# Optimization experiments

Hardware: AMD Instinct MI355X
Metric: run time of the kernel (lower is better)

The kernel has to match this reference:

```python
import jax, jax.numpy as jnp
import numpy as np

# Per-species MLP dims from CoefficientLayer._create_model (H, C, N, O), aev_dim=384
DIMS = {"h": [384, 160, 128, 96, 1], "c": [384, 144, 112, 96, 1], "n": [384, 128, 112, 96, 1], "o": [384, 128, 112, 96, 1]}


def setup_inputs() -> dict:
    key = jax.random.key(0)
    B, A, D = 256, 256, 384
    ks = jax.random.split(key, 64)
    inp = {}
    inp["species"] = jax.random.randint(ks[0], (B, A), 0, 4)  # species index 0..3
    inp["aev"] = jax.random.normal(ks[1], (B, A, D), dtype=jnp.float32)
    inp["b0"] = jnp.array([0.1, 0.2, 0.3, 0.4], dtype=jnp.float32)  # shifter intercepts
    inp["b1"] = jnp.array([1.0, 1.1, 0.9, 1.2], dtype=jnp.float32)  # shifter slopes
    ki = 2
    for name, dims in DIMS.items():
        for l in range(4):
            fi, fo = dims[l], dims[l + 1]
            inp[f"{name}w{l}"] = jax.random.normal(ks[ki], (fi, fo), dtype=jnp.float32) / np.float32(np.sqrt(fi))
            ki += 1
            inp[f"{name}b{l}"] = jnp.zeros((fo,), dtype=jnp.float32)
    return inp


def _mlp(x, ws, bs):
    # Linear -> CELU(0.1) x3 -> Linear(->1), squeeze last dim
    for i in range(3):
        x = jax.nn.celu(x @ ws[i] + bs[i], alpha=0.1)
    return (x @ ws[3] + bs[3])[..., 0]


def reference(species, aev, b0, b1,
              hw0, hb0, hw1, hb1, hw2, hb2, hw3, hb3,
              cw0, cb0, cw1, cb1, cw2, cb2, cw3, cb3,
              nw0, nb0, nw1, nb1, nw2, nb2, nw3, nb3,
              ow0, ob0, ow1, ob1, ow2, ob2, ow3, ob3):
    nets = [
        ([hw0, hw1, hw2, hw3], [hb0, hb1, hb2, hb3]),
        ([cw0, cw1, cw2, cw3], [cb0, cb1, cb2, cb3]),
        ([nw0, nw1, nw2, nw3], [nb0, nb1, nb2, nb3]),
        ([ow0, ow1, ow2, ow3], [ob0, ob1, ob2, ob3]),
    ]
    # ANIModel hard routing: each atom's coefficient comes from its species' network;
    # atoms with species == -1 (padding) stay 0.
    coef = jnp.zeros(species.shape, dtype=aev.dtype)
    for i, (ws, bs) in enumerate(nets):  # fixed small loop over 4 species
        coef = jnp.where(species == i, _mlp(aev, ws, bs), coef)
    # Shifter: result[mask_i] = b0[i] + b1[i] * coef[mask_i]; padding stays 0
    idx = jnp.clip(species, 0)
    return jnp.where(species >= 0, b0[idx] + b1[idx] * coef, jnp.zeros((), dtype=aev.dtype))
```

## Files before the change

### kernel.cpp

```cpp
#include <hip/hip_runtime.h>

typedef _Float16 f16;
typedef _Float16 f16x8 __attribute__((ext_vector_type(8)));
typedef float f32x4 __attribute__((ext_vector_type(4)));
typedef unsigned short u16;

#define NATOMS 65536
#define SLOT 10240

#define WS_LISTS_OFF 256
#define WS_W_OFF 524544
#define WS_W_ELEMS 350208
#define WS_NEEDED (WS_W_OFF + WS_W_ELEMS * 2)

struct ConvJob { const float* src; int K, N, KS, NT, CK, off; };

struct PrepParams {
  const int* species;
  int* counts;
  u16* lists;
  f16* wbase;
  ConvJob jobs[16];
};

struct MlpParams {
  const float* aev;
  const float* b0;
  const float* b1;
  const float* bias[4][4];
  const f16* w[4][4];
  const int* counts;
  const u16* lists;
  float* out;
  int Nreal0[4];
  int Nreal1[4];
};

__global__ __launch_bounds__(256) void prep_kernel(PrepParams p) {
  int tid = threadIdx.x;
  if (blockIdx.x < 256) {
    __shared__ int wcnt[4][4];
    __shared__ int wbase[4][4];
    int i = blockIdx.x * 256 + tid;
    int s = p.species[i];
    int wave = tid >> 6, lane = tid & 63;
    unsigned long long m[4];
    #pragma unroll
    for (int t = 0; t < 4; t++) {
      m[t] = __ballot(s == t);
      if (lane == 0) wcnt[wave][t] = __popcll(m[t]);
    }
    __syncthreads();
    if (tid < 4) {
      int t = tid;
      int c0 = wcnt[0][t], c1 = wcnt[1][t], c2 = wcnt[2][t], c3 = wcnt[3][t];
      int base = atomicAdd(&p.counts[t], c0 + c1 + c2 + c3);
      wbase[0][t] = base;
      wbase[1][t] = base + c0;
      wbase[2][t] = base + c0 + c1;
      wbase[3][t] = base + c0 + c1 + c2;
    }
    __syncthreads();
    int rnk = __popcll(m[s] & ((1ull << lane) - 1ull));
    p.lists[s * NATOMS + wbase[wave][s] + rnk] = (u16)i;
  } else {
    int bx = blockIdx.x - 256;
    int job = bx / 30, bxin = bx - job * 30;
    ConvJob jb = p.jobs[job];
    int e = bxin * 256 + tid;
    int nslots = jb.KS * jb.NT * 64;
    if (e >= nslots) return;
    int frag = e >> 6, lane = e & 63;
    int c = frag / (jb.CK * jb.NT);
    int rem = frag - c * (jb.CK * jb.NT);
    int ckc = min(jb.CK, jb.KS - c * jb.CK);
    int nt = rem / ckc, ki = rem - nt * ckc;
    int ks = c * jb.CK + ki;
    int q = lane >> 4, nlo = lane & 15;
    int n = nt * 16 + nlo;
    int k0 = ks * 32 + q * 8;
    f16x8 v;
    #pragma unroll
    for (int j = 0; j < 8; j++) {
      int k = k0 + j;
      float x = (n < jb.N && k < jb.K) ? jb.src[k * jb.N + n] : 0.f;
      v[j] = (f16)x;
    }
    *(f16x8*)(p.wbase + jb.off + (size_t)e * 8) = v;
  }
}

__device__ __forceinline__ float celu01(float v) {
  return v > 0.f ? v : 0.1f * (__expf(v * 10.f) - 1.f);
}

__device__ __forceinline__ void stage_frag(const f16* g, f16* l, int lane) {
  __builtin_amdgcn_global_load_lds(
      (const __attribute__((address_space(1))) unsigned int*)(g + lane * 8),
      (__attribute__((address_space(3))) unsigned int*)l, 16, 0, 0);
}

template <int KS, int NT, int CK>
__device__ __forceinline__ int run_layer(const f16x8* a, const f16* __restrict__ Wt,
                                         const float* __restrict__ bias, int Nreal,
                                         f16* dstw, int DS, f16* ring, int par,
                                         const f16* nextW, int nextNF,
                                         f32x4* acc, int w, int lane, int q, int nlo) {
  constexpr int C = (KS + CK - 1) / CK;
  #pragma unroll
  for (int nt = 0; nt < NT; nt++) acc[nt] = f32x4{0.f, 0.f, 0.f, 0.f};
  #pragma unroll
  for (int c = 0; c < C; c++) {
    f16* cur = ring + par * SLOT;
    f16* nxt = ring + (par ^ 1) * SLOT;
    if (c + 1 < C) {
      const f16* gb = Wt + (size_t)((c + 1) * CK * NT) * 512;
      int nf = min(CK, KS - (c + 1) * CK) * NT;
      for (int f = w; f < nf; f += 4)
        stage_frag(gb + (size_t)f * 512, nxt + f * 512, lane);
    } else if (nextNF > 0) {
      for (int f = w; f < nextNF; f += 4)
        stage_frag(nextW + (size_t)f * 512, nxt + f * 512, lane);
    }
    int ckc = min(CK, KS - c * CK);
    #pragma unroll
    for (int nt = 0; nt < NT; nt++) {
      #pragma unroll
      for (int ki = 0; ki < CK; ki++) {
        if (ki < ckc) {
          f16x8 b = *(const f16x8*)(cur + (nt * ckc + ki) * 512 + lane * 8);
          acc[nt] = __builtin_amdgcn_mfma_f32_16x16x32_f16(a[c * CK + ki], b, acc[nt], 0, 0, 0);
        }
      }
    }
    __syncthreads();
    par ^= 1;
  }
  #pragma unroll
  for (int nt = 0; nt < NT; nt++) {
    int n = nt * 16 + nlo;
    float bv = (n < Nreal) ? bias[n] : 0.f;
    #pragma unroll
    for (int r = 0; r < 4; r++) {
      float v = celu01(acc[nt][r] + bv);
      dstw[(q * 4 + r) * DS + n] = (f16)v;
    }
  }
  return par;
}

template <int NT0, int KS1>
__device__ __forceinline__ void mlp_body(const MlpParams& p, int s, int tile,
                                         f16* ring, f16* Bf0, f16* Bf1) {
  int cnt = p.counts[s];
  if (tile * 64 >= cnt) return;
  const u16* list = p.lists + s * NATOMS;
  int tid = threadIdx.x, w = tid >> 6, lane = tid & 63;
  int q = lane >> 4, nlo = lane & 15;
  int rowbase = tile * 64 + w * 16;
  int atom = list[min(rowbase + nlo, cnt - 1)];

  f16x8 a0[12];
  const float* ap = p.aev + (size_t)atom * 384 + q * 8;
  #pragma unroll
  for (int ks = 0; ks < 12; ks++) {
    float4 u0 = *(const float4*)(ap + ks * 32);
    float4 u1 = *(const float4*)(ap + ks * 32 + 4);
    f16x8 t = {(f16)u0.x, (f16)u0.y, (f16)u0.z, (f16)u0.w,
               (f16)u1.x, (f16)u1.y, (f16)u1.z, (f16)u1.w};
    a0[ks] = t;
  }

  for (int f = w; f < 2 * NT0; f += 4)
    stage_frag(p.w[s][0] + (size_t)f * 512, ring + f * 512, lane);
  __syncthreads();

  f16* my0 = Bf0 + (w * 16) * 168;
  f16* my1 = Bf1 + (w * 16) * 136;
  f32x4 acc[10];

  int par = 0;
  par = run_layer<12, NT0, 2>(a0, p.w[s][0], p.bias[s][0], p.Nreal0[s], my0, 168,
                              ring, par, p.w[s][1], 16, acc, w, lane, q, nlo);

  f16x8 a1[KS1];
  #pragma unroll
  for (int ks = 0; ks < KS1; ks++)
    a1[ks] = *(const f16x8*)(my0 + nlo * 168 + ks * 32 + q * 8);
  par = run_layer<KS1, 8, 2>(a1, p.w[s][1], p.bias[s][1], p.Nreal1[s], my1, 136,
                             ring, par, p.w[s][2], 12, acc, w, lane, q, nlo);

  f16x8 a2[4];
  #pragma unroll
  for (int ks = 0; ks < 4; ks++)
    a2[ks] = *(const f16x8*)(my1 + nlo * 136 + ks * 32 + q * 8);
  par = run_layer<4, 6, 2>(a2, p.w[s][2], p.bias[s][2], 96, my0, 168,
                           ring, par, (const f16*)0, 0, acc, w, lane, q, nlo);

  f16x8 a3[3];
  #pragma unroll
  for (int ks = 0; ks < 3; ks++)
    a3[ks] = *(const f16x8*)(my0 + nlo * 168 + ks * 32 + q * 8);
  f32x4 acc3 = {0.f, 0.f, 0.f, 0.f};
  const f16* W3 = p.w[s][3];
  #pragma unroll
  for (int ks = 0; ks < 3; ks++) {
    f16x8 b = *(const f16x8*)(W3 + (size_t)(ks * 64 + lane) * 8);
    acc3 = __builtin_amdgcn_mfma_f32_16x16x32_f16(a3[ks], b, acc3, 0, 0, 0);
  }
  if (nlo == 0) {
    float b3 = p.bias[s][3][0];
    float b0v = p.b0[s], b1v = p.b1[s];
    #pragma unroll
    for (int r = 0; r < 4; r++) {
      int m = rowbase + q * 4 + r;
      if (m < cnt) {
        float coef = acc3[r] + b3;
        p.out[list[m]] = b0v + b1v * coef;
      }
    }
  }
}

__global__ __launch_bounds__(256, 2) void mlp_kernel(MlpParams p) {
  __shared__ f16 ring[2 * SLOT];
  __shared__ f16 Bf0[64 * 168];
  __shared__ f16 Bf1[64 * 136];
  int s = blockIdx.x & 3;
  int tile = blockIdx.x >> 2;
  switch (s) {
    case 0: mlp_body<10, 5>(p, 0, tile, ring, Bf0, Bf1); break;
    case 1: mlp_body<10, 5>(p, 1, tile, ring, Bf0, Bf1); break;
    case 2: mlp_body<8, 4>(p, 2, tile, ring, Bf0, Bf1); break;
    default: mlp_body<8, 4>(p, 3, tile, ring, Bf0, Bf1); break;
  }
}

extern "C" void kernel_launch(void* const* d_in, const int* in_sizes, int n_in,
                              void* d_out, int out_size, void* d_ws, size_t ws_size,
                              hipStream_t stream) {
  if (ws_size < WS_NEEDED) return;

  const int* species = (const int*)d_in[0];
  const float* aev = (const float*)d_in[1];
  const float* b0 = (const float*)d_in[2];
  const float* b1 = (const float*)d_in[3];

  static const int F1[4]  = {160, 144, 128, 128};
  static const int F1p[4] = {160, 160, 128, 128};
  static const int F2[4]  = {128, 112, 112, 112};

  char* wsb = (char*)d_ws;
  int* counts = (int*)wsb;
  u16* lists = (u16*)(wsb + WS_LISTS_OFF);
  f16* wbase = (f16*)(wsb + WS_W_OFF);

  PrepParams pp;
  pp.species = species; pp.counts = counts; pp.lists = lists; pp.wbase = wbase;

  MlpParams mp;
  mp.aev = aev; mp.b0 = b0; mp.b1 = b1;
  mp.counts = counts; mp.lists = lists; mp.out = (float*)d_out;

  int off = 0, ji = 0;
  for (int s = 0; s < 4; s++) {
    int K[4]  = {384, F1[s], F2[s], 96};
    int N[4]  = {F1[s], F2[s], 96, 1};
    int KS[4] = {12, F1p[s] / 32, 4, 3};
    int NT[4] = {F1p[s] / 16, 8, 6, 1};
    int CK[4] = {2, 2, 2, 3};
    for (int l = 0; l < 4; l++) {
      const float* w = (const float*)d_in[4 + s * 8 + l * 2];
      const float* b = (const float*)d_in[4 + s * 8 + l * 2 + 1];
      pp.jobs[ji].src = w;
      pp.jobs[ji].K = K[l];
      pp.jobs[ji].N = N[l];
      pp.jobs[ji].KS = KS[l];
      pp.jobs[ji].NT = NT[l];
      pp.jobs[ji].CK = CK[l];
      pp.jobs[ji].off = off;
      mp.w[s][l] = wbase + off;
      mp.bias[s][l] = b;
      off += KS[l] * NT[l] * 512;
      ji++;
    }
    mp.Nreal0[s] = F1[s];
    mp.Nreal1[s] = F2[s];
  }

  hipMemsetAsync(d_ws, 0, 64, stream);
  prep_kernel<<<dim3(256 + 480), 256, 0, stream>>>(pp);
  mlp_kernel<<<dim3(280 * 4), 256, 0, stream>>>(mp);
}
```

Measured before the change: 284.1 us.

## Warp-specialize weight staging with a producer wave and flag-synced triple-buffered ring

Adds a dedicated fifth wave that streams all layer weight chunks into a three-slot LDS ring via async global-to-LDS loads, signalling consumers through shared flags and waiting on per-chunk completion counters instead of block-wide barriers. Consumer waves process one K-step per chunk and merge the two activation buffers into one, shrinking LDS to allow more resident blocks. This aims to remove __syncthreads stalls and overlap weight loading across layer boundaries, at the cost of spin-wait polling, atomics, and finer-grained chunks.

```diff
diff --git a/kernel.cpp b/kernel.cpp
--- a/kernel.cpp
+++ b/kernel.cpp
@@ -6,7 +6,8 @@
 typedef unsigned short u16;
 
 #define NATOMS 65536
-#define SLOT 10240
+#define SLOT 5120
+#define RING 3
 
 #define WS_LISTS_OFF 256
 #define WS_W_OFF 524544
@@ -100,41 +101,69 @@
       (__attribute__((address_space(3))) unsigned int*)l, 16, 0, 0);
 }
 
-template <int KS, int NT, int CK>
-__device__ __forceinline__ int run_layer(const f16x8* a, const f16* __restrict__ Wt,
-                                         const float* __restrict__ bias, int Nreal,
-                                         f16* dstw, int DS, f16* ring, int par,
-                                         const f16* nextW, int nextNF,
-                                         f32x4* acc, int w, int lane, int q, int nlo) {
-  constexpr int C = (KS + CK - 1) / CK;
+template <int NT0, int KS1>
+struct Sched {
+  static constexpr int NC = 12 + KS1 + 4 + 1;
+  static constexpr int frags(int c) {
+    return c < 12 ? NT0 : (c < 12 + KS1 ? 8 : (c < 12 + KS1 + 4 ? 6 : 3));
+  }
+};
+
+template <int NT0, int KS1, int C>
+__device__ __forceinline__ void issue_chunk(const f16* w0, const f16* w1,
+                                            const f16* w2, const f16* w3,
+                                            f16* ring, int lane) {
+  constexpr int NF = Sched<NT0, KS1>::frags(C);
+  const f16* g;
+  if constexpr (C < 12) g = w0 + (size_t)C * NT0 * 512;
+  else if constexpr (C < 12 + KS1) g = w1 + (size_t)(C - 12) * 8 * 512;
+  else if constexpr (C < 12 + KS1 + 4) g = w2 + (size_t)(C - 12 - KS1) * 6 * 512;
+  else g = w3;
+  f16* l = ring + (C % RING) * SLOT;
+  #pragma unroll
+  for (int f = 0; f < NF; f++)
+    stage_frag(g + f * 512, l + f * 512, lane);
+}
+
+template <int NT0, int KS1, int C>
+__device__ void prod_step(const f16* w0, const f16* w1, const f16* w2, const f16* w3,
+                          f16* ring, volatile int* flag, volatile int* done, int lane) {
+  constexpr int NC = Sched<NT0, KS1>::NC;
+  constexpr int NXT = (C + 1 < NC) ? Sched<NT0, KS1>::frags(C + 1) : 0;
+  __builtin_amdgcn_s_waitcnt((NXT & 15) | ((NXT >> 4) << 14) | 0x0F70);
+  __asm__ volatile("" ::: "memory");
+  if (lane == 0) flag[C] = 1;
+  if constexpr (C + 2 < NC) {
+    if constexpr (C >= 1) {
+      while (done[C - 1] < 4) __builtin_amdgcn_s_sleep(1);
+      __asm__ volatile("" ::: "memory");
+    }
+    issue_chunk<NT0, KS1, C + 2>(w0, w1, w2, w3, ring, lane);
+  }
+  if constexpr (C + 1 < NC)
+    prod_step<NT0, KS1, C + 1>(w0, w1, w2, w3, ring, flag, done, lane);
+}
+
+template <int KS, int NT, int CB, bool ACT>
+__device__ __forceinline__ void consume_layer(const f16x8* a, const f16* ring,
+                                              volatile int* flag, int* done,
+                                              const float* __restrict__ bias, int Nreal,
+                                              f16* dstw, int lane, int q, int nlo) {
+  f32x4 acc[NT];
   #pragma unroll
   for (int nt = 0; nt < NT; nt++) acc[nt] = f32x4{0.f, 0.f, 0.f, 0.f};
   #pragma unroll
-  for (int c = 0; c < C; c++) {
-    f16* cur = ring + par * SLOT;
-    f16* nxt = ring + (par ^ 1) * SLOT;
-    if (c + 1 < C) {
-      const f16* gb = Wt + (size_t)((c + 1) * CK * NT) * 512;
-      int nf = min(CK, KS - (c + 1) * CK) * NT;
-      for (int f = w; f < nf; f += 4)
-        stage_frag(gb + (size_t)f * 512, nxt + f * 512, lane);
-    } else if (nextNF > 0) {
-      for (int f = w; f < nextNF; f += 4)
-        stage_frag(nextW + (size_t)f * 512, nxt + f * 512, lane);
-    }
-    int ckc = min(CK, KS - c * CK);
+  for (int c = 0; c < KS; c++) {
+    while (flag[CB + c] == 0) __builtin_amdgcn_s_sleep(1);
+    __asm__ volatile("" ::: "memory");
+    const f16* slot = ring + ((CB + c) % RING) * SLOT;
     #pragma unroll
     for (int nt = 0; nt < NT; nt++) {
-      #pragma unroll
-      for (int ki = 0; ki < CK; ki++) {
-        if (ki < ckc) {
-          f16x8 b = *(const f16x8*)(cur + (nt * ckc + ki) * 512 + lane * 8);
-          acc[nt] = __builtin_amdgcn_mfma_f32_16x16x32_f16(a[c * CK + ki], b, acc[nt], 0, 0, 0);
-        }
-      }
-    }
-    __syncthreads();
-    par ^= 1;
+      f16x8 b = *(const f16x8*)(slot + nt * 512 + lane * 8);
+      acc[nt] = __builtin_amdgcn_mfma_f32_16x16x32_f16(a[c], b, acc[nt], 0, 0, 0);
+    }
+    __asm__ volatile("" ::: "memory");
+    if (lane == 0) atomicAdd(&done[CB + c], 1);
   }
   #pragma unroll
   for (int nt = 0; nt < NT; nt++) {
@@ -142,20 +171,32 @@
     float bv = (n < Nreal) ? bias[n] : 0.f;
     #pragma unroll
     for (int r = 0; r < 4; r++) {
-      float v = celu01(acc[nt][r] + bv);
-      dstw[(q * 4 + r) * DS + n] = (f16)v;
-    }
-  }
-  return par;
+      float v = acc[nt][r] + bv;
+      if (ACT) v = celu01(v);
+      dstw[(q * 4 + r) * 168 + n] = (f16)v;
+    }
+  }
 }
 
 template <int NT0, int KS1>
 __device__ __forceinline__ void mlp_body(const MlpParams& p, int s, int tile,
-                                         f16* ring, f16* Bf0, f16* Bf1) {
+                                         f16* ring, f16* Bf, int* flag, int* done) {
   int cnt = p.counts[s];
   if (tile * 64 >= cnt) return;
+  int tid = threadIdx.x, w = tid >> 6, lane = tid & 63;
+  if (tid < 24) flag[tid] = 0;
+  else if (tid < 48) done[tid - 24] = 0;
+  __syncthreads();
+
+  if (w == 4) {
+    const f16 *w0 = p.w[s][0], *w1 = p.w[s][1], *w2 = p.w[s][2], *w3 = p.w[s][3];
+    issue_chunk<NT0, KS1, 0>(w0, w1, w2, w3, ring, lane);
+    issue_chunk<NT0, KS1, 1>(w0, w1, w2, w3, ring, lane);
+    prod_step<NT0, KS1, 0>(w0, w1, w2, w3, ring, (volatile int*)flag, (volatile int*)done, lane);
+    return;
+  }
+
   const u16* list = p.lists + s * NATOMS;
-  int tid = threadIdx.x, w = tid >> 6, lane = tid & 63;
   int q = lane >> 4, nlo = lane & 15;
   int rowbase = tile * 64 + w * 16;
   int atom = list[min(rowbase + nlo, cnt - 1)];
@@ -171,41 +212,36 @@
     a0[ks] = t;
   }
 
-  for (int f = w; f < 2 * NT0; f += 4)
-    stage_frag(p.w[s][0] + (size_t)f * 512, ring + f * 512, lane);
-  __syncthreads();
-
-  f16* my0 = Bf0 + (w * 16) * 168;
-  f16* my1 = Bf1 + (w * 16) * 136;
-  f32x4 acc[10];
-
-  int par = 0;
-  par = run_layer<12, NT0, 2>(a0, p.w[s][0], p.bias[s][0], p.Nreal0[s], my0, 168,
-                              ring, par, p.w[s][1], 16, acc, w, lane, q, nlo);
-
+  volatile int* vflag = (volatile int*)flag;
+  f16* my = Bf + (w * 16) * 168;
+
+  consume_layer<12, NT0, 0, true>(a0, ring, vflag, done, p.bias[s][0], p.Nreal0[s],
+                                  my, lane, q, nlo);
   f16x8 a1[KS1];
   #pragma unroll
   for (int ks = 0; ks < KS1; ks++)
-    a1[ks] = *(const f16x8*)(my0 + nlo * 168 + ks * 32 + q * 8);
-  par = run_layer<KS1, 8, 2>(a1, p.w[s][1], p.bias[s][1], p.Nreal1[s], my1, 136,
-                             ring, par, p.w[s][2], 12, acc, w, lane, q, nlo);
-
+    a1[ks] = *(const f16x8*)(my + nlo * 168 + ks * 32 + q * 8);
+  consume_layer<KS1, 8, 12, true>(a1, ring, vflag, done, p.bias[s][1], p.Nreal1[s],
+                                  my, lane, q, nlo);
   f16x8 a2[4];
   #pragma unroll
   for (int ks = 0; ks < 4; ks++)
-    a2[ks] = *(const f16x8*)(my1 + nlo * 136 + ks * 32 + q * 8);
-  par = run_layer<4, 6, 2>(a2, p.w[s][2], p.bias[s][2], 96, my0, 168,
-                           ring, par, (const f16*)0, 0, acc, w, lane, q, nlo);
+    a2[ks] = *(const f16x8*)(my + nlo * 168 + ks * 32 + q * 8);
+  consume_layer<4, 6, 12 + KS1, true>(a2, ring, vflag, done, p.bias[s][2], 96,
+                                      my, lane, q, nlo);
 
   f16x8 a3[3];
   #pragma unroll
   for (int ks = 0; ks < 3; ks++)
-    a3[ks] = *(const f16x8*)(my0 + nlo * 168 + ks * 32 + q * 8);
+    a3[ks] = *(const f16x8*)(my + nlo * 168 + ks * 32 + q * 8);
+  constexpr int G3 = 12 + KS1 + 4;
+  while (vflag[G3] == 0) __builtin_amdgcn_s_sleep(1);
+  __asm__ volatile("" ::: "memory");
+  const f16* slot = ring + (G3 % RING) * SLOT;
   f32x4 acc3 = {0.f, 0.f, 0.f, 0.f};
-  const f16* W3 = p.w[s][3];
   #pragma unroll
   for (int ks = 0; ks < 3; ks++) {
-    f16x8 b = *(const f16x8*)(W3 + (size_t)(ks * 64 + lane) * 8);
+    f16x8 b = *(const f16x8*)(slot + ks * 512 + lane * 8);
     acc3 = __builtin_amdgcn_mfma_f32_16x16x32_f16(a3[ks], b, acc3, 0, 0, 0);
   }
   if (nlo == 0) {
@@ -222,17 +258,18 @@
   }
 }
 
-__global__ __launch_bounds__(256, 2) void mlp_kernel(MlpParams p) {
-  __shared__ f16 ring[2 * SLOT];
-  __shared__ f16 Bf0[64 * 168];
-  __shared__ f16 Bf1[64 * 136];
+__global__ __launch_bounds__(320, 3) void mlp_kernel(MlpParams p) {
+  __shared__ f16 ring[RING * SLOT];
+  __shared__ f16 Bf[64 * 168];
+  __shared__ int flag[24];
+  __shared__ int done[24];
   int s = blockIdx.x & 3;
   int tile = blockIdx.x >> 2;
   switch (s) {
-    case 0: mlp_body<10, 5>(p, 0, tile, ring, Bf0, Bf1); break;
-    case 1: mlp_body<10, 5>(p, 1, tile, ring, Bf0, Bf1); break;
-    case 2: mlp_body<8, 4>(p, 2, tile, ring, Bf0, Bf1); break;
-    default: mlp_body<8, 4>(p, 3, tile, ring, Bf0, Bf1); break;
+    case 0: mlp_body<10, 5>(p, 0, tile, ring, Bf, flag, done); break;
+    case 1: mlp_body<10, 5>(p, 1, tile, ring, Bf, flag, done); break;
+    case 2: mlp_body<8, 4>(p, 2, tile, ring, Bf, flag, done); break;
+    default: mlp_body<8, 4>(p, 3, tile, ring, Bf, flag, done); break;
   }
 }
 
@@ -268,7 +305,7 @@
     int N[4]  = {F1[s], F2[s], 96, 1};
     int KS[4] = {12, F1p[s] / 32, 4, 3};
     int NT[4] = {F1p[s] / 16, 8, 6, 1};
-    int CK[4] = {2, 2, 2, 3};
+    int CK[4] = {1, 1, 1, 3};
     for (int l = 0; l < 4; l++) {
       const float* w = (const float*)d_in[4 + s * 8 + l * 2];
       const float* b = (const float*)d_in[4 + s * 8 + l * 2 + 1];
@@ -290,5 +327,5 @@
 
   hipMemsetAsync(d_ws, 0, 64, stream);
   prep_kernel<<<dim3(256 + 480), 256, 0, stream>>>(pp);
-  mlp_kernel<<<dim3(280 * 4), 256, 0, stream>>>(mp);
-}
+  mlp_kernel<<<dim3(280 * 4), 320, 0, stream>>>(mp);
+}
```

New measurement: 273.5 us. 3.7% less time.

## Read MLP weight fragments directly from global memory instead of LDS ring staging

Applied to the files above, without the earlier changes.

Removes the double-buffered LDS ring that staged weight fragments with global_load_lds, along with its per-chunk __syncthreads. Each wave now loads B fragments straight from global memory, relying on L2 to serve them, and computes two N-tiles at a time. The weight layout is changed so each N-tile holds all of its K-slices contiguously. Activations now use a single shared buffer reused in place, which shrinks LDS use enough to allow 4 blocks per CU. The trade-off is that every wave fetches the weights itself, so cache traffic rises in exchange for dropping the barriers and raising occupancy.

```diff
diff --git a/kernel.cpp b/kernel.cpp
--- a/kernel.cpp
+++ b/kernel.cpp
@@ -6,7 +6,6 @@
 typedef unsigned short u16;
 
 #define NATOMS 65536
-#define SLOT 10240
 
 #define WS_LISTS_OFF 256
 #define WS_W_OFF 524544
@@ -94,64 +93,51 @@
   return v > 0.f ? v : 0.1f * (__expf(v * 10.f) - 1.f);
 }
 
-__device__ __forceinline__ void stage_frag(const f16* g, f16* l, int lane) {
-  __builtin_amdgcn_global_load_lds(
-      (const __attribute__((address_space(1))) unsigned int*)(g + lane * 8),
-      (__attribute__((address_space(3))) unsigned int*)l, 16, 0, 0);
-}
-
-template <int KS, int NT, int CK>
-__device__ __forceinline__ int run_layer(const f16x8* a, const f16* __restrict__ Wt,
-                                         const float* __restrict__ bias, int Nreal,
-                                         f16* dstw, int DS, f16* ring, int par,
-                                         const f16* nextW, int nextNF,
-                                         f32x4* acc, int w, int lane, int q, int nlo) {
-  constexpr int C = (KS + CK - 1) / CK;
-  #pragma unroll
-  for (int nt = 0; nt < NT; nt++) acc[nt] = f32x4{0.f, 0.f, 0.f, 0.f};
-  #pragma unroll
-  for (int c = 0; c < C; c++) {
-    f16* cur = ring + par * SLOT;
-    f16* nxt = ring + (par ^ 1) * SLOT;
-    if (c + 1 < C) {
-      const f16* gb = Wt + (size_t)((c + 1) * CK * NT) * 512;
-      int nf = min(CK, KS - (c + 1) * CK) * NT;
-      for (int f = w; f < nf; f += 4)
-        stage_frag(gb + (size_t)f * 512, nxt + f * 512, lane);
-    } else if (nextNF > 0) {
-      for (int f = w; f < nextNF; f += 4)
-        stage_frag(nextW + (size_t)f * 512, nxt + f * 512, lane);
-    }
-    int ckc = min(CK, KS - c * CK);
-    #pragma unroll
-    for (int nt = 0; nt < NT; nt++) {
+template <int KS, int K>
+struct Duo {
+  template <int KA>
+  static __device__ __forceinline__ void go(const f16x8 (&a)[KA], f32x4& c0, f32x4& c1,
+                                            const f16* __restrict__ b0,
+                                            const f16* __restrict__ b1, int lane) {
+    if constexpr (K < KS) {
+      f16x8 x0 = *(const f16x8*)(b0 + (size_t)K * 512 + lane * 8);
+      f16x8 x1 = *(const f16x8*)(b1 + (size_t)K * 512 + lane * 8);
+      c0 = __builtin_amdgcn_mfma_f32_16x16x32_f16(a[K], x0, c0, 0, 0, 0);
+      c1 = __builtin_amdgcn_mfma_f32_16x16x32_f16(a[K], x1, c1, 0, 0, 0);
+      Duo<KS, K + 1>::go(a, c0, c1, b0, b1, lane);
+    }
+  }
+};
+
+template <int KS, int NT, bool ACT, int NTI = 0>
+struct Layer {
+  template <int KA>
+  static __device__ __forceinline__ void go(const f16x8 (&a)[KA],
+                                            const f16* __restrict__ W,
+                                            const float* __restrict__ bias, int Nreal,
+                                            f16* dstw, int lane, int q, int nlo) {
+    if constexpr (NTI < NT) {
+      f32x4 c0 = {0.f, 0.f, 0.f, 0.f}, c1 = {0.f, 0.f, 0.f, 0.f};
+      const f16* b0 = W + (size_t)(NTI * KS) * 512;
+      const f16* b1 = b0 + (size_t)KS * 512;
+      Duo<KS, 0>::go(a, c0, c1, b0, b1, lane);
+      int n0 = NTI * 16 + nlo, n1 = n0 + 16;
+      float bv0 = (n0 < Nreal) ? bias[n0] : 0.f;
+      float bv1 = (n1 < Nreal) ? bias[n1] : 0.f;
       #pragma unroll
-      for (int ki = 0; ki < CK; ki++) {
-        if (ki < ckc) {
-          f16x8 b = *(const f16x8*)(cur + (nt * ckc + ki) * 512 + lane * 8);
-          acc[nt] = __builtin_amdgcn_mfma_f32_16x16x32_f16(a[c * CK + ki], b, acc[nt], 0, 0, 0);
-        }
+      for (int r = 0; r < 4; r++) {
+        float v0 = c0[r] + bv0, v1 = c1[r] + bv1;
+        if (ACT) { v0 = celu01(v0); v1 = celu01(v1); }
+        dstw[(q * 4 + r) * 168 + n0] = (f16)v0;
+        dstw[(q * 4 + r) * 168 + n1] = (f16)v1;
       }
-    }
-    __syncthreads();
-    par ^= 1;
-  }
-  #pragma unroll
-  for (int nt = 0; nt < NT; nt++) {
-    int n = nt * 16 + nlo;
-    float bv = (n < Nreal) ? bias[n] : 0.f;
-    #pragma unroll
-    for (int r = 0; r < 4; r++) {
-      float v = celu01(acc[nt][r] + bv);
-      dstw[(q * 4 + r) * DS + n] = (f16)v;
-    }
-  }
-  return par;
-}
+      Layer<KS, NT, ACT, NTI + 2>::go(a, W, bias, Nreal, dstw, lane, q, nlo);
+    }
+  }
+};
 
 template <int NT0, int KS1>
-__device__ __forceinline__ void mlp_body(const MlpParams& p, int s, int tile,
-                                         f16* ring, f16* Bf0, f16* Bf1) {
+__device__ __forceinline__ void mlp_body(const MlpParams& p, int s, int tile, f16* Bf) {
   int cnt = p.counts[s];
   if (tile * 64 >= cnt) return;
   const u16* list = p.lists + s * NATOMS;
@@ -171,41 +157,31 @@
     a0[ks] = t;
   }
 
-  for (int f = w; f < 2 * NT0; f += 4)
-    stage_frag(p.w[s][0] + (size_t)f * 512, ring + f * 512, lane);
-  __syncthreads();
-
-  f16* my0 = Bf0 + (w * 16) * 168;
-  f16* my1 = Bf1 + (w * 16) * 136;
-  f32x4 acc[10];
-
-  int par = 0;
-  par = run_layer<12, NT0, 2>(a0, p.w[s][0], p.bias[s][0], p.Nreal0[s], my0, 168,
-                              ring, par, p.w[s][1], 16, acc, w, lane, q, nlo);
+  f16* my = Bf + (w * 16) * 168;
+
+  Layer<12, NT0, true>::go(a0, p.w[s][0], p.bias[s][0], p.Nreal0[s], my, lane, q, nlo);
 
   f16x8 a1[KS1];
   #pragma unroll
   for (int ks = 0; ks < KS1; ks++)
-    a1[ks] = *(const f16x8*)(my0 + nlo * 168 + ks * 32 + q * 8);
-  par = run_layer<KS1, 8, 2>(a1, p.w[s][1], p.bias[s][1], p.Nreal1[s], my1, 136,
-                             ring, par, p.w[s][2], 12, acc, w, lane, q, nlo);
+    a1[ks] = *(const f16x8*)(my + nlo * 168 + ks * 32 + q * 8);
+  Layer<KS1, 8, true>::go(a1, p.w[s][1], p.bias[s][1], p.Nreal1[s], my, lane, q, nlo);
 
   f16x8 a2[4];
   #pragma unroll
   for (int ks = 0; ks < 4; ks++)
-    a2[ks] = *(const f16x8*)(my1 + nlo * 136 + ks * 32 + q * 8);
-  par = run_layer<4, 6, 2>(a2, p.w[s][2], p.bias[s][2], 96, my0, 168,
-                           ring, par, (const f16*)0, 0, acc, w, lane, q, nlo);
+    a2[ks] = *(const f16x8*)(my + nlo * 168 + ks * 32 + q * 8);
+  Layer<4, 6, true>::go(a2, p.w[s][2], p.bias[s][2], 96, my, lane, q, nlo);
 
   f16x8 a3[3];
   #pragma unroll
   for (int ks = 0; ks < 3; ks++)
-    a3[ks] = *(const f16x8*)(my0 + nlo * 168 + ks * 32 + q * 8);
+    a3[ks] = *(const f16x8*)(my + nlo * 168 + ks * 32 + q * 8);
   f32x4 acc3 = {0.f, 0.f, 0.f, 0.f};
   const f16* W3 = p.w[s][3];
   #pragma unroll
   for (int ks = 0; ks < 3; ks++) {
-    f16x8 b = *(const f16x8*)(W3 + (size_t)(ks * 64 + lane) * 8);
+    f16x8 b = *(const f16x8*)(W3 + (size_t)ks * 512 + lane * 8);
     acc3 = __builtin_amdgcn_mfma_f32_16x16x32_f16(a3[ks], b, acc3, 0, 0, 0);
   }
   if (nlo == 0) {
@@ -222,17 +198,15 @@
   }
 }
 
-__global__ __launch_bounds__(256, 2) void mlp_kernel(MlpParams p) {
-  __shared__ f16 ring[2 * SLOT];
-  __shared__ f16 Bf0[64 * 168];
-  __shared__ f16 Bf1[64 * 136];
+__global__ __launch_bounds__(256, 4) void mlp_kernel(MlpParams p) {
+  __shared__ f16 Bf[64 * 168];
   int s = blockIdx.x & 3;
   int tile = blockIdx.x >> 2;
   switch (s) {
-    case 0: mlp_body<10, 5>(p, 0, tile, ring, Bf0, Bf1); break;
-    case 1: mlp_body<10, 5>(p, 1, tile, ring, Bf0, Bf1); break;
-    case 2: mlp_body<8, 4>(p, 2, tile, ring, Bf0, Bf1); break;
-    default: mlp_body<8, 4>(p, 3, tile, ring, Bf0, Bf1); break;
+    case 0: mlp_body<10, 5>(p, 0, tile, Bf); break;
+    case 1: mlp_body<10, 5>(p, 1, tile, Bf); break;
+    case 2: mlp_body<8, 4>(p, 2, tile, Bf); break;
+    default: mlp_body<8, 4>(p, 3, tile, Bf); break;
   }
 }
 
@@ -268,7 +242,6 @@
     int N[4]  = {F1[s], F2[s], 96, 1};
     int KS[4] = {12, F1p[s] / 32, 4, 3};
     int NT[4] = {F1p[s] / 16, 8, 6, 1};
-    int CK[4] = {2, 2, 2, 3};
     for (int l = 0; l < 4; l++) {
       const float* w = (const float*)d_in[4 + s * 8 + l * 2];
       const float* b = (const float*)d_in[4 + s * 8 + l * 2 + 1];
@@ -277,7 +250,7 @@
       pp.jobs[ji].N = N[l];
       pp.jobs[ji].KS = KS[l];
       pp.jobs[ji].NT = NT[l];
-      pp.jobs[ji].CK = CK[l];
+      pp.jobs[ji].CK = KS[l];
       pp.jobs[ji].off = off;
       mp.w[s][l] = wbase + off;
       mp.bias[s][l] = b;
```

After: 274.4 us. 1.04x faster.
